# Kernel tuning notes

Measured on AMD Instinct MI355X. Metric: run time of the kernel, lower is better.

Reference implementation:

```python
import jax, jax.numpy as jnp
import numpy as np

B, S, D, H, BLK = 2, 4096, 1024, 16, 64

def setup_inputs() -> dict:
    key = jax.random.key(0)
    ks = jax.random.split(key, 6)
    sc = 0.02
    nb = S // BLK
    g_tok = 128
    ng = g_tok // BLK
    n_mid = nb - ng - 2
    return {
        "tokens": jax.random.normal(ks[0], (B, S, D), dtype=jnp.float32),
        "band_mask": jnp.ones((B, 1, n_mid, BLK, 3 * BLK), dtype=jnp.float32),
        "from_mask": jnp.ones((B, 1, S, 1), dtype=jnp.float32),
        "to_mask": jnp.ones((B, 1, 1, S), dtype=jnp.float32),
        "Wq": jax.random.normal(ks[1], (D, D), dtype=jnp.float32) * sc,
        "Wk": jax.random.normal(ks[2], (D, D), dtype=jnp.float32) * sc,
        "Wv": jax.random.normal(ks[3], (D, D), dtype=jnp.float32) * sc,
        "Wu": jax.random.normal(ks[4], (D, D), dtype=jnp.float32) * sc,
        "bu": jnp.zeros((D,), dtype=jnp.float32),
        "num_global_tokens": 128,
    }

def _forward(tokens, band_mask, from_mask, to_mask, Wq, Wk, Wv, Wu, bu, g):
    b, s, dm = tokens.shape
    h, blk = H, BLK
    d = dm // h
    nb = s // blk
    ng = g // blk
    rs = 1.0 / (d ** 0.5)
    pen = -10000.0

    def heads(x):
        return x.reshape(b, s, h, d).transpose(0, 2, 1, 3)  # (b,h,s,d)

    q = heads(tokens @ Wq)
    k = heads(tokens @ Wk)
    v = heads(tokens @ Wv)
    bq = q.reshape(b, h, nb, blk, d)
    bk = k.reshape(b, h, nb, blk, d)
    bv = v.reshape(b, h, nb, blk, d)

    # --- global (first) block rows: attend to everything ---
    fp = jnp.einsum('bhqd,bhkd->bhqk', q[:, :, :g], k) * rs + (1.0 - to_mask) * pen
    fw = jax.nn.softmax(fp, axis=-1)
    first = jnp.einsum('bhqk,bhkd->bhqd', fw, v).reshape(b, h, ng, blk, d)

    # --- second block: global keys + first 3 non-global blocks ---
    q1 = min(3, nb - ng)
    st = ng * blk
    k2 = jnp.concatenate([k[:, :, :g], k[:, :, st:st + q1 * blk]], axis=2)
    v2 = jnp.concatenate([v[:, :, :g], v[:, :, st:st + q1 * blk]], axis=2)
    p2 = jnp.einsum('bhqd,bhkd->bhqk', bq[:, :, ng], k2) * rs
    p2 = p2 + (1.0 - to_mask[:, :, :, :blk * (ng + q1)]) * pen
    c2 = jnp.einsum('bhqk,bhkd->bhqd', jax.nn.softmax(p2, axis=-1), v2)[:, :, None]

    # --- middle blocks: sliding window (prev, self, next) + global keys ---
    m = nb - ng - 2
    ek = jnp.concatenate([bk[:, :, ng:ng + m], bk[:, :, ng + 1:ng + 1 + m],
                          bk[:, :, ng + 2:ng + 2 + m]], axis=3)  # (b,h,m,3*blk,d)
    ev = jnp.concatenate([bv[:, :, ng:ng + m], bv[:, :, ng + 1:ng + 1 + m],
                          bv[:, :, ng + 2:ng + 2 + m]], axis=3)
    mq = bq[:, :, ng + 1:ng + 1 + m]  # (b,h,m,blk,d)
    inner = jnp.einsum('bhmqd,bhmkd->bhmqk', mq, ek) * rs + (1.0 - band_mask) * pen
    fb = jnp.einsum('bhmqd,bhkd->bhmqk', mq, k[:, :, :g]) * rs
    fb = fb + (1.0 - to_mask[:, :, :, :g][:, :, :, None, :]) * pen
    aw = jax.nn.softmax(jnp.concatenate([fb, inner], axis=-1), axis=-1)
    cm = (jnp.einsum('bhmqk,bhmkd->bhmqd', aw[..., g:], ev)
          + jnp.einsum('bhmqk,bhkd->bhmqd', aw[..., :g], v[:, :, :g]))

    # --- last block: global keys + last 3 blocks ---
    ql = min(3, nb - ng)
    kl = jnp.concatenate([k[:, :, :g], k[:, :, -(ql * blk):]], axis=2)
    vl = jnp.concatenate([v[:, :, :g], v[:, :, -(ql * blk):]], axis=2)
    lm = jnp.concatenate([to_mask[:, :, :, :g], to_mask[:, :, :, -(ql * blk):]], axis=3)
    pl = jnp.einsum('bhqd,bhkd->bhqk', bq[:, :, -1], kl) * rs + (1.0 - lm) * pen
    cl = jnp.einsum('bhqk,bhkd->bhqd', jax.nn.softmax(pl, axis=-1), vl)[:, :, None]

    ctx = jnp.concatenate([first, c2, cm, cl], axis=2).reshape(b, h, s, d) * from_mask
    ctx = ctx.transpose(0, 2, 1, 3).reshape(b, s, dm)
    return ctx @ Wu + bu

def reference(tokens, band_mask, from_mask, to_mask, Wq, Wk, Wv, Wu, bu, num_global_tokens):
    return _forward(tokens, band_mask, from_mask, to_mask, Wq, Wk, Wv, Wu, bu, num_global_tokens)
```

## Files before the change

### kernel.cpp

```cpp
#include <hip/hip_runtime.h>

typedef unsigned short u16;
using bfrag = __attribute__((ext_vector_type(8))) short;
using f32x4 = __attribute__((ext_vector_type(4))) float;

#define PEN  (-10000.0f)
#define RSC  (0.125f)

__device__ __forceinline__ u16 f2bf(float f) {
  union { float f; unsigned u; } v; v.f = f;
  unsigned r = v.u + 0x7fffu + ((v.u >> 16) & 1u);
  return (u16)(r >> 16);
}

__device__ __forceinline__ void gload16(const u16* g, u16* l) {
  __builtin_amdgcn_global_load_lds(
      (const __attribute__((address_space(1))) unsigned int*)g,
      (__attribute__((address_space(3))) unsigned int*)l, 16, 0, 0);
}

__global__ __launch_bounds__(256) void prep_k(
    const float* __restrict__ tokens, u16* __restrict__ tok_bf,
    const float* __restrict__ w0, const float* __restrict__ w1,
    const float* __restrict__ w2, const float* __restrict__ w3,
    u16* __restrict__ wt) {
  __shared__ float tile[64][65];
  int id = blockIdx.x, t = threadIdx.x;
  if (id < 8192) {
    int i = id * 256 + t;
    float4 v = ((const float4*)tokens)[i];
    u16 o[4] = { f2bf(v.x), f2bf(v.y), f2bf(v.z), f2bf(v.w) };
    *(uint2*)(tok_bf + (size_t)i * 4) = *(uint2*)o;
    return;
  }
  int wid = id - 8192;
  int z = wid >> 8, rem = wid & 255;
  const float* W = (z == 0) ? w0 : (z == 1) ? w1 : (z == 2) ? w2 : w3;
  u16* out = wt + (size_t)z * 1024 * 1024;
  int k0 = (rem & 15) * 64, n0 = (rem >> 4) * 64;
#pragma unroll
  for (int i = 0; i < 16; ++i) {
    int idx = i * 256 + t, kk = idx >> 6, nn = idx & 63;
    tile[nn][kk] = W[(size_t)(k0 + kk) * 1024 + n0 + nn];
  }
  __syncthreads();
#pragma unroll
  for (int i = 0; i < 16; ++i) {
    int idx = i * 256 + t, nn = idx >> 6, kk = idx & 63;
    out[(size_t)(n0 + nn) * 1024 + k0 + kk] = f2bf(tile[nn][kk]);
  }
}

__global__ __launch_bounds__(256) void gemm_qkv_k(
    const u16* __restrict__ A, const u16* __restrict__ WT,
    u16* __restrict__ Q, u16* __restrict__ K, u16* __restrict__ VT) {
  __shared__ alignas(16) u16 smem[17408];
  u16* As = smem;
  u16* Bs = smem + 8192;
  int t = threadIdx.x;
  int n0 = blockIdx.x * 128, r0 = blockIdx.y * 128;
  int wave = t >> 6, lane = t & 63, quad = lane >> 4, lcol = lane & 15;
  int wr = wave & 1, wc = wave >> 1;
  int rsel = lane >> 3;
  int sseg = (lane & 7) ^ rsel;
  f32x4 acc[4][4];
#pragma unroll
  for (int mt = 0; mt < 4; ++mt)
#pragma unroll
    for (int nt = 0; nt < 4; ++nt) acc[mt][nt] = (f32x4){0.f, 0.f, 0.f, 0.f};

  const u16* a0 = A + (size_t)r0 * 1024 + sseg * 8;
  const u16* b0 = WT + (size_t)n0 * 1024 + sseg * 8;
  int sw = lcol & 7;

  for (int kt = 0; kt < 16; ++kt) {
#pragma unroll
    for (int i = 0; i < 4; ++i) {
      int ii = wave * 4 + i;
      int row = ii * 8 + rsel;
      gload16(a0 + (size_t)row * 1024 + kt * 64, As + ii * 512);
      gload16(b0 + (size_t)row * 1024 + kt * 64, Bs + ii * 512);
    }
    __syncthreads();
#pragma unroll
    for (int kh = 0; kh < 2; ++kh) {
      int seg = ((kh * 4 + quad) ^ sw) * 8;
      bfrag af[4], bf[4];
#pragma unroll
      for (int x = 0; x < 4; ++x) {
        af[x] = *(const bfrag*)(As + (wr * 64 + x * 16 + lcol) * 64 + seg);
        bf[x] = *(const bfrag*)(Bs + (wc * 64 + x * 16 + lcol) * 64 + seg);
      }
#pragma unroll
      for (int mt = 0; mt < 4; ++mt)
#pragma unroll
        for (int nt = 0; nt < 4; ++nt)
          acc[mt][nt] = __builtin_amdgcn_mfma_f32_16x16x32_bf16(af[mt], bf[nt], acc[mt][nt], 0, 0, 0);
    }
    __syncthreads();
  }
  u16 (*Cs)[136] = (u16(*)[136])smem;
#pragma unroll
  for (int mt = 0; mt < 4; ++mt)
#pragma unroll
    for (int nt = 0; nt < 4; ++nt)
#pragma unroll
      for (int r = 0; r < 4; ++r)
        Cs[wr * 64 + mt * 16 + quad * 4 + r][wc * 64 + nt * 16 + lcol] = f2bf(acc[mt][nt][r]);
  __syncthreads();
  int which = n0 >> 10;
  int b = r0 >> 12, s0v = r0 & 4095;
  if (which < 2) {
    int row = t >> 1, seg = t & 1;
    int h = ((n0 & 1023) >> 6) + seg;
    u16* outp = (which == 0 ? Q : K) + (((size_t)(b * 16 + h) * 4096 + s0v + row) << 6);
#pragma unroll
    for (int jj = 0; jj < 8; ++jj)
      *(uint4*)(outp + jj * 8) = *(uint4*)&Cs[row][seg * 64 + jj * 8];
  } else {
    int c = t & 127, h = ((n0 & 1023) >> 6) + (c >> 6), d = c & 63;
    u16* vtrow = VT + ((size_t)(b * 16 + h) << 18) + ((size_t)d << 12) + s0v;
    int sgb = t >> 7;
#pragma unroll
    for (int i = 0; i < 8; ++i) {
      int sg = sgb + 2 * i;
      u16 tmp[8];
#pragma unroll
      for (int rr = 0; rr < 8; ++rr) tmp[rr] = Cs[sg * 8 + rr][c];
      *(uint4*)(vtrow + sg * 8) = *(uint4*)tmp;
    }
  }
}

__global__ __launch_bounds__(256) void attn_band_k(
    const u16* __restrict__ Qg, const u16* __restrict__ Kg, const u16* __restrict__ VTg,
    const float* __restrict__ band_mask, const float* __restrict__ from_mask,
    const float* __restrict__ to_mask, u16* __restrict__ ctx) {
  __shared__ alignas(16) u16 Qs[64][72];
  __shared__ alignas(16) u16 Ks[64][72];
  __shared__ alignas(16) u16 VTs[64][72];
  __shared__ alignas(16) u16 Ps[64][72];

  int t = threadIdx.x;
  int wave = t >> 6, lane = t & 63, quad = lane >> 4, lcol = lane & 15;
  int j = blockIdx.x + 2, bh = blockIdx.y, b = bh >> 4;

  const u16* qsrc = Qg + (((size_t)bh * 4096 + j * 64) << 6);
#pragma unroll
  for (int i = 0; i < 2; ++i) {
    int idx = i * 256 + t, row = idx >> 3, c8 = (idx & 7) << 3;
    *(uint4*)&Qs[row][c8] = *(const uint4*)(qsrc + row * 64 + c8);
  }
  __syncthreads();
  bfrag qf[2];
#pragma unroll
  for (int kh = 0; kh < 2; ++kh)
    qf[kh] = *(const bfrag*)&Qs[wave * 16 + lcol][kh * 32 + quad * 8];

  float l_part[4] = {0.f, 0.f, 0.f, 0.f};
  f32x4 oa[4];
#pragma unroll
  for (int nt = 0; nt < 4; ++nt) oa[nt] = (f32x4){0.f, 0.f, 0.f, 0.f};

  int sb = (j == 2) ? 2 : ((j == 63) ? 61 : j - 1);

  for (int it = 0; it < 5; ++it) {
    int kb = (it < 2) ? it : (sb + it - 2);
    const u16* ksrc = Kg + (((size_t)bh * 4096 + kb * 64) << 6);
    const u16* vsrc = VTg + ((size_t)bh << 18) + kb * 64;
#pragma unroll
    for (int i = 0; i < 2; ++i) {
      int idx = i * 256 + t, row = idx >> 3, c8 = (idx & 7) << 3;
      *(uint4*)&Ks[row][c8] = *(const uint4*)(ksrc + row * 64 + c8);
      *(uint4*)&VTs[row][c8] = *(const uint4*)(vsrc + ((size_t)row << 12) + c8);
    }
    __syncthreads();

    f32x4 sc[4];
#pragma unroll
    for (int nt = 0; nt < 4; ++nt) sc[nt] = (f32x4){0.f, 0.f, 0.f, 0.f};
#pragma unroll
    for (int kh = 0; kh < 2; ++kh) {
      int kc = kh * 32 + quad * 8;
#pragma unroll
      for (int nt = 0; nt < 4; ++nt) {
        bfrag kf = *(const bfrag*)&Ks[nt * 16 + lcol][kc];
        sc[nt] = __builtin_amdgcn_mfma_f32_16x16x32_bf16(qf[kh], kf, sc[nt], 0, 0, 0);
      }
    }

    bool band = (j >= 3) && (j <= 62) && (it >= 2);
    if (!band) {
#pragma unroll
      for (int nt = 0; nt < 4; ++nt) {
        float tm = to_mask[b * 4096 + kb * 64 + nt * 16 + lcol];
        float pn = (1.0f - tm) * PEN;
#pragma unroll
        for (int r = 0; r < 4; ++r) {
          float p = __expf(sc[nt][r] * RSC + pn);
          l_part[r] += p;
          Ps[wave * 16 + quad * 4 + r][nt * 16 + lcol] = f2bf(p);
        }
      }
    } else {
      const float* bm = band_mask + (((size_t)b * 60 + (j - 3)) << 6) * 192 + (it - 2) * 64;
#pragma unroll
      for (int r = 0; r < 4; ++r) {
        int qrow = wave * 16 + quad * 4 + r;
#pragma unroll
        for (int nt = 0; nt < 4; ++nt) {
          float msk = bm[(size_t)qrow * 192 + nt * 16 + lcol];
          float p = __expf(sc[nt][r] * RSC + (1.0f - msk) * PEN);
          l_part[r] += p;
          Ps[qrow][nt * 16 + lcol] = f2bf(p);
        }
      }
    }
    __syncthreads();

#pragma unroll
    for (int kh = 0; kh < 2; ++kh) {
      bfrag pf = *(const bfrag*)&Ps[wave * 16 + lcol][kh * 32 + quad * 8];
#pragma unroll
      for (int nt = 0; nt < 4; ++nt) {
        bfrag vf = *(const bfrag*)&VTs[nt * 16 + lcol][kh * 32 + quad * 8];
        oa[nt] = __builtin_amdgcn_mfma_f32_16x16x32_bf16(pf, vf, oa[nt], 0, 0, 0);
      }
    }
    __syncthreads();
  }

  float sc_r[4];
#pragma unroll
  for (int r = 0; r < 4; ++r) {
#pragma unroll
    for (int d = 1; d < 16; d <<= 1) l_part[r] += __shfl_xor(l_part[r], d);
    int qrow = wave * 16 + quad * 4 + r;
    sc_r[r] = from_mask[b * 4096 + j * 64 + qrow] / l_part[r];
  }
#pragma unroll
  for (int nt = 0; nt < 4; ++nt)
#pragma unroll
    for (int r = 0; r < 4; ++r)
      Qs[wave * 16 + quad * 4 + r][nt * 16 + lcol] = f2bf(oa[nt][r] * sc_r[r]);
  __syncthreads();
  u16* dst = ctx + (((size_t)bh * 4096 + j * 64) << 6);
#pragma unroll
  for (int i = 0; i < 2; ++i) {
    int idx = i * 256 + t, row = idx >> 3, c8 = (idx & 7) << 3;
    *(uint4*)(dst + row * 64 + c8) = *(uint4*)&Qs[row][c8];
  }
}

__global__ __launch_bounds__(256) void attn_global_k(
    const u16* __restrict__ Qg, const u16* __restrict__ Kg, const u16* __restrict__ VTg,
    const float* __restrict__ to_mask,
    float* __restrict__ Opart, float* __restrict__ lbuf) {
  __shared__ alignas(16) u16 Qs[64][72];
  __shared__ alignas(16) u16 Ks[64][72];
  __shared__ alignas(16) u16 VTs[64][72];
  __shared__ alignas(16) u16 Ps[64][72];

  int t = threadIdx.x;
  int wave = t >> 6, lane = t & 63, quad = lane >> 4, lcol = lane & 15;
  int jc = blockIdx.x, j = jc >> 3, chunk = jc & 7;
  int bh = blockIdx.y, b = bh >> 4;

  const u16* qsrc = Qg + (((size_t)bh * 4096 + j * 64) << 6);
#pragma unroll
  for (int i = 0; i < 2; ++i) {
    int idx = i * 256 + t, row = idx >> 3, c8 = (idx & 7) << 3;
    *(uint4*)&Qs[row][c8] = *(const uint4*)(qsrc + row * 64 + c8);
  }
  __syncthreads();
  bfrag qf[2];
#pragma unroll
  for (int kh = 0; kh < 2; ++kh)
    qf[kh] = *(const bfrag*)&Qs[wave * 16 + lcol][kh * 32 + quad * 8];

  float l_part[4] = {0.f, 0.f, 0.f, 0.f};
  f32x4 oa[4];
#pragma unroll
  for (int nt = 0; nt < 4; ++nt) oa[nt] = (f32x4){0.f, 0.f, 0.f, 0.f};

  for (int it = 0; it < 8; ++it) {
    int kb = chunk * 8 + it;
    const u16* ksrc = Kg + (((size_t)bh * 4096 + kb * 64) << 6);
    const u16* vsrc = VTg + ((size_t)bh << 18) + kb * 64;
#pragma unroll
    for (int i = 0; i < 2; ++i) {
      int idx = i * 256 + t, row = idx >> 3, c8 = (idx & 7) << 3;
      *(uint4*)&Ks[row][c8] = *(const uint4*)(ksrc + row * 64 + c8);
      *(uint4*)&VTs[row][c8] = *(const uint4*)(vsrc + ((size_t)row << 12) + c8);
    }
    __syncthreads();

    f32x4 sc[4];
#pragma unroll
    for (int nt = 0; nt < 4; ++nt) sc[nt] = (f32x4){0.f, 0.f, 0.f, 0.f};
#pragma unroll
    for (int kh = 0; kh < 2; ++kh) {
      int kc = kh * 32 + quad * 8;
#pragma unroll
      for (int nt = 0; nt < 4; ++nt) {
        bfrag kf = *(const bfrag*)&Ks[nt * 16 + lcol][kc];
        sc[nt] = __builtin_amdgcn_mfma_f32_16x16x32_bf16(qf[kh], kf, sc[nt], 0, 0, 0);
      }
    }

#pragma unroll
    for (int nt = 0; nt < 4; ++nt) {
      float tm = to_mask[b * 4096 + kb * 64 + nt * 16 + lcol];
      float pn = (1.0f - tm) * PEN;
#pragma unroll
      for (int r = 0; r < 4; ++r) {
        float p = __expf(sc[nt][r] * RSC + pn);
        l_part[r] += p;
        Ps[wave * 16 + quad * 4 + r][nt * 16 + lcol] = f2bf(p);
      }
    }
    __syncthreads();

#pragma unroll
    for (int kh = 0; kh < 2; ++kh) {
      bfrag pf = *(const bfrag*)&Ps[wave * 16 + lcol][kh * 32 + quad * 8];
#pragma unroll
      for (int nt = 0; nt < 4; ++nt) {
        bfrag vf = *(const bfrag*)&VTs[nt * 16 + lcol][kh * 32 + quad * 8];
        oa[nt] = __builtin_amdgcn_mfma_f32_16x16x32_bf16(pf, vf, oa[nt], 0, 0, 0);
      }
    }
    __syncthreads();
  }

  size_t base = (((size_t)(bh * 2 + j) * 8 + chunk) << 6);
#pragma unroll
  for (int nt = 0; nt < 4; ++nt)
#pragma unroll
    for (int r = 0; r < 4; ++r) {
      int row = wave * 16 + quad * 4 + r;
      Opart[((base + row) << 6) + nt * 16 + lcol] = oa[nt][r];
    }
#pragma unroll
  for (int r = 0; r < 4; ++r) {
#pragma unroll
    for (int d = 1; d < 16; d <<= 1) l_part[r] += __shfl_xor(l_part[r], d);
  }
  if (lcol == 0) {
#pragma unroll
    for (int r = 0; r < 4; ++r) {
      int row = wave * 16 + quad * 4 + r;
      lbuf[base + row] = l_part[r];
    }
  }
}

__global__ __launch_bounds__(256) void attn_combine_k(
    const float* __restrict__ Opart, const float* __restrict__ lbuf,
    const float* __restrict__ from_mask, u16* __restrict__ ctx) {
  int blk = blockIdx.x;
  int bh = blk >> 1, j = blk & 1, b = bh >> 4;
  int t = threadIdx.x;
  int row = t >> 2, dseg = (t & 3) << 4;

  float lt = 0.0f;
  float acc[16];
#pragma unroll
  for (int u = 0; u < 16; ++u) acc[u] = 0.0f;
#pragma unroll
  for (int c = 0; c < 8; ++c) {
    size_t rbase = (((size_t)blk * 8 + c) << 6) + row;
    lt += lbuf[rbase];
    const float* op = Opart + (rbase << 6) + dseg;
#pragma unroll
    for (int u = 0; u < 4; ++u) {
      float4 v = *(const float4*)(op + u * 4);
      acc[u * 4 + 0] += v.x;
      acc[u * 4 + 1] += v.y;
      acc[u * 4 + 2] += v.z;
      acc[u * 4 + 3] += v.w;
    }
  }
  float inv = from_mask[b * 4096 + j * 64 + row] / lt;
  u16* dst = ctx + (((size_t)bh * 4096 + j * 64 + row) << 6) + dseg;
  u16 o[8];
#pragma unroll
  for (int u = 0; u < 8; ++u) o[u] = f2bf(acc[u] * inv);
  *(uint4*)dst = *(uint4*)o;
#pragma unroll
  for (int u = 0; u < 8; ++u) o[u] = f2bf(acc[8 + u] * inv);
  *(uint4*)(dst + 8) = *(uint4*)o;
}

__global__ __launch_bounds__(256) void gemm_out_k(
    const u16* __restrict__ ctx, const u16* __restrict__ WTu,
    const float* __restrict__ bu, float* __restrict__ out) {
  __shared__ alignas(16) u16 smem[16384];
  u16* As = smem;
  u16* Bs = smem + 8192;
  int t = threadIdx.x;
  int n0 = blockIdx.x * 128, r0 = blockIdx.y * 128;
  int wave = t >> 6, lane = t & 63, quad = lane >> 4, lcol = lane & 15;
  int wr = wave & 1, wc = wave >> 1;
  int b = r0 >> 12, s0 = r0 & 4095;
  int rsel = lane >> 3;
  int sseg = (lane & 7) ^ rsel;
  int sw = lcol & 7;
  f32x4 acc[4][4];
#pragma unroll
  for (int mt = 0; mt < 4; ++mt)
#pragma unroll
    for (int nt = 0; nt < 4; ++nt) acc[mt][nt] = (f32x4){0.f, 0.f, 0.f, 0.f};

  const u16* b0 = WTu + (size_t)n0 * 1024 + sseg * 8;
  for (int kt = 0; kt < 16; ++kt) {
    const u16* a0 = ctx + (((size_t)(b * 16 + kt) * 4096 + s0) << 6) + sseg * 8;
#pragma unroll
    for (int i = 0; i < 4; ++i) {
      int ii = wave * 4 + i;
      int row = ii * 8 + rsel;
      gload16(a0 + (size_t)row * 64, As + ii * 512);
      gload16(b0 + (size_t)row * 1024 + kt * 64, Bs + ii * 512);
    }
    __syncthreads();
#pragma unroll
    for (int kh = 0; kh < 2; ++kh) {
      int seg = ((kh * 4 + quad) ^ sw) * 8;
      bfrag af[4], bf[4];
#pragma unroll
      for (int x = 0; x < 4; ++x) {
        af[x] = *(const bfrag*)(As + (wr * 64 + x * 16 + lcol) * 64 + seg);
        bf[x] = *(const bfrag*)(Bs + (wc * 64 + x * 16 + lcol) * 64 + seg);
      }
#pragma unroll
      for (int mt = 0; mt < 4; ++mt)
#pragma unroll
        for (int nt = 0; nt < 4; ++nt)
          acc[mt][nt] = __builtin_amdgcn_mfma_f32_16x16x32_bf16(af[mt], bf[nt], acc[mt][nt], 0, 0, 0);
    }
    __syncthreads();
  }
#pragma unroll
  for (int nt = 0; nt < 4; ++nt) {
    int n = n0 + wc * 64 + nt * 16 + lcol;
    float bv = bu[n];
#pragma unroll
    for (int mt = 0; mt < 4; ++mt)
#pragma unroll
      for (int r = 0; r < 4; ++r)
        out[(size_t)(r0 + wr * 64 + mt * 16 + quad * 4 + r) * 1024 + n] = acc[mt][nt][r] + bv;
  }
}

extern "C" void kernel_launch(void* const* d_in, const int* in_sizes, int n_in,
                              void* d_out, int out_size, void* d_ws, size_t ws_size,
                              hipStream_t stream) {
  const float* tokens    = (const float*)d_in[0];
  const float* band_mask = (const float*)d_in[1];
  const float* from_mask = (const float*)d_in[2];
  const float* to_mask   = (const float*)d_in[3];
  const float* Wq = (const float*)d_in[4];
  const float* Wk = (const float*)d_in[5];
  const float* Wv = (const float*)d_in[6];
  const float* Wu = (const float*)d_in[7];
  const float* bu = (const float*)d_in[8];
  float* out = (float*)d_out;

  char* ws = (char*)d_ws;
  u16* tok_bf = (u16*)(ws);
  u16* WT     = (u16*)(ws + 16777216);
  u16* Qb     = (u16*)(ws + 16777216 + 8388608);
  u16* Kb     = Qb + 8388608;
  u16* VTb    = Kb + 8388608;
  u16* ctx    = VTb + 8388608;
  float* Opart = (float*)(ctx + 8388608);
  float* lb    = Opart + (size_t)32 * 2 * 8 * 64 * 64;

  prep_k<<<9216, 256, 0, stream>>>(tokens, tok_bf, Wq, Wk, Wv, Wu, WT);
  gemm_qkv_k<<<dim3(24, 64), 256, 0, stream>>>(tok_bf, WT, Qb, Kb, VTb);
  attn_band_k<<<dim3(62, 32), 256, 0, stream>>>(Qb, Kb, VTb, band_mask, from_mask, to_mask, ctx);
  attn_global_k<<<dim3(16, 32), 256, 0, stream>>>(Qb, Kb, VTb, to_mask, Opart, lb);
  attn_combine_k<<<64, 256, 0, stream>>>(Opart, lb, from_mask, ctx);
  gemm_out_k<<<dim3(8, 64), 256, 0, stream>>>(ctx, WT + (size_t)3 * 1024 * 1024, bu, out);
}
```

Before: 261.7 us.

## Merge band and global attention kernels with double-buffered async K/V loads

Fuses the band and global attention kernels into a single launch, choosing the role from the block index. K and V^T tiles are now double-buffered and fetched with global_load_lds direct-to-LDS loads so the next tile streams in while the current one is computed. Shared memory uses an XOR swizzle instead of padding, and the Q and P buffers share one allocation. This removes a kernel launch and the load stall at each iteration, at the cost of more complex indexing and extra LDS for the second buffer.

```diff
diff --git a/kernel.cpp b/kernel.cpp
--- a/kernel.cpp
+++ b/kernel.cpp
@@ -132,65 +132,92 @@
   }
 }
 
-__global__ __launch_bounds__(256) void attn_band_k(
+__global__ __launch_bounds__(256) void attn_k(
     const u16* __restrict__ Qg, const u16* __restrict__ Kg, const u16* __restrict__ VTg,
     const float* __restrict__ band_mask, const float* __restrict__ from_mask,
-    const float* __restrict__ to_mask, u16* __restrict__ ctx) {
-  __shared__ alignas(16) u16 Qs[64][72];
-  __shared__ alignas(16) u16 Ks[64][72];
-  __shared__ alignas(16) u16 VTs[64][72];
-  __shared__ alignas(16) u16 Ps[64][72];
+    const float* __restrict__ to_mask, u16* __restrict__ ctx,
+    float* __restrict__ Opart, float* __restrict__ lbuf) {
+  __shared__ alignas(16) u16 QPs[4096];
+  __shared__ alignas(16) u16 Ks[2][4096];
+  __shared__ alignas(16) u16 VTs[2][4096];
 
   int t = threadIdx.x;
   int wave = t >> 6, lane = t & 63, quad = lane >> 4, lcol = lane & 15;
-  int j = blockIdx.x + 2, bh = blockIdx.y, b = bh >> 4;
-
-  const u16* qsrc = Qg + (((size_t)bh * 4096 + j * 64) << 6);
-#pragma unroll
-  for (int i = 0; i < 2; ++i) {
-    int idx = i * 256 + t, row = idx >> 3, c8 = (idx & 7) << 3;
-    *(uint4*)&Qs[row][c8] = *(const uint4*)(qsrc + row * 64 + c8);
-  }
+  int rsel = lane >> 3, sseg = (lane & 7) ^ rsel;
+  int sw = lcol & 7;
+  int bh = blockIdx.y, b = bh >> 4;
+  bool is_band = blockIdx.x < 62;
+  int j, chunk = 0, nit, sb = 0;
+  if (is_band) {
+    j = blockIdx.x + 2; nit = 5;
+    sb = (j == 2) ? 2 : ((j == 63) ? 61 : j - 1);
+  } else {
+    int jc = blockIdx.x - 62; j = jc >> 3; chunk = jc & 7; nit = 8;
+  }
+  bool bandmask_blk = is_band && (j >= 3) && (j <= 62);
+
+  const u16* kbase = Kg + (((size_t)bh * 4096) << 6) + sseg * 8;
+  const u16* vbase = VTg + ((size_t)bh << 18) + sseg * 8;
+
+  auto kb_of = [&](int it) {
+    return is_band ? ((it < 2) ? it : (sb + it - 2)) : (chunk * 8 + it);
+  };
+  auto stage = [&](int kb, int buf) {
+#pragma unroll
+    for (int i = 0; i < 2; ++i) {
+      int ii = wave * 2 + i;
+      int row = ii * 8 + rsel;
+      gload16(kbase + (((size_t)kb * 64 + row) << 6), &Ks[buf][ii * 512]);
+      gload16(vbase + ((size_t)row << 12) + kb * 64, &VTs[buf][ii * 512]);
+    }
+  };
+
+  {
+    const u16* qsrc = Qg + (((size_t)bh * 4096 + j * 64) << 6) + sseg * 8;
+#pragma unroll
+    for (int i = 0; i < 2; ++i) {
+      int ii = wave * 2 + i;
+      gload16(qsrc + (ii * 8 + rsel) * 64, &QPs[ii * 512]);
+    }
+  }
+  stage(kb_of(0), 0);
   __syncthreads();
+
   bfrag qf[2];
 #pragma unroll
   for (int kh = 0; kh < 2; ++kh)
-    qf[kh] = *(const bfrag*)&Qs[wave * 16 + lcol][kh * 32 + quad * 8];
+    qf[kh] = *(const bfrag*)&QPs[(wave * 16 + lcol) * 64 + ((kh * 4 + quad) ^ sw) * 8];
+  __syncthreads();
 
   float l_part[4] = {0.f, 0.f, 0.f, 0.f};
   f32x4 oa[4];
 #pragma unroll
   for (int nt = 0; nt < 4; ++nt) oa[nt] = (f32x4){0.f, 0.f, 0.f, 0.f};
 
-  int sb = (j == 2) ? 2 : ((j == 63) ? 61 : j - 1);
-
-  for (int it = 0; it < 5; ++it) {
-    int kb = (it < 2) ? it : (sb + it - 2);
-    const u16* ksrc = Kg + (((size_t)bh * 4096 + kb * 64) << 6);
-    const u16* vsrc = VTg + ((size_t)bh << 18) + kb * 64;
-#pragma unroll
-    for (int i = 0; i < 2; ++i) {
-      int idx = i * 256 + t, row = idx >> 3, c8 = (idx & 7) << 3;
-      *(uint4*)&Ks[row][c8] = *(const uint4*)(ksrc + row * 64 + c8);
-      *(uint4*)&VTs[row][c8] = *(const uint4*)(vsrc + ((size_t)row << 12) + c8);
-    }
-    __syncthreads();
+  int poff = lcol & 7;
+  int hb = lcol >> 3;
+  int q1_4 = (quad & 1) * 4;
+
+  for (int it = 0; it < nit; ++it) {
+    int buf = it & 1;
+    if (it + 1 < nit) stage(kb_of(it + 1), buf ^ 1);
+    int kb = kb_of(it);
 
     f32x4 sc[4];
 #pragma unroll
     for (int nt = 0; nt < 4; ++nt) sc[nt] = (f32x4){0.f, 0.f, 0.f, 0.f};
 #pragma unroll
     for (int kh = 0; kh < 2; ++kh) {
-      int kc = kh * 32 + quad * 8;
+      int seg = ((kh * 4 + quad) ^ sw) * 8;
 #pragma unroll
       for (int nt = 0; nt < 4; ++nt) {
-        bfrag kf = *(const bfrag*)&Ks[nt * 16 + lcol][kc];
+        bfrag kf = *(const bfrag*)&Ks[buf][(nt * 16 + lcol) * 64 + seg];
         sc[nt] = __builtin_amdgcn_mfma_f32_16x16x32_bf16(qf[kh], kf, sc[nt], 0, 0, 0);
       }
     }
 
-    bool band = (j >= 3) && (j <= 62) && (it >= 2);
-    if (!band) {
+    bool use_band = bandmask_blk && (it >= 2);
+    if (!use_band) {
 #pragma unroll
       for (int nt = 0; nt < 4; ++nt) {
         float tm = to_mask[b * 4096 + kb * 64 + nt * 16 + lcol];
@@ -199,7 +226,8 @@
         for (int r = 0; r < 4; ++r) {
           float p = __expf(sc[nt][r] * RSC + pn);
           l_part[r] += p;
-          Ps[wave * 16 + quad * 4 + r][nt * 16 + lcol] = f2bf(p);
+          int pseg = (nt * 2 + hb) ^ (q1_4 + r);
+          QPs[(wave * 16 + quad * 4 + r) * 64 + pseg * 8 + poff] = f2bf(p);
         }
       }
     } else {
@@ -212,7 +240,8 @@
           float msk = bm[(size_t)qrow * 192 + nt * 16 + lcol];
           float p = __expf(sc[nt][r] * RSC + (1.0f - msk) * PEN);
           l_part[r] += p;
-          Ps[qrow][nt * 16 + lcol] = f2bf(p);
+          int pseg = (nt * 2 + hb) ^ (q1_4 + r);
+          QPs[qrow * 64 + pseg * 8 + poff] = f2bf(p);
         }
       }
     }
@@ -220,137 +249,58 @@
 
 #pragma unroll
     for (int kh = 0; kh < 2; ++kh) {
-      bfrag pf = *(const bfrag*)&Ps[wave * 16 + lcol][kh * 32 + quad * 8];
+      int seg = ((kh * 4 + quad) ^ sw) * 8;
+      bfrag pf = *(const bfrag*)&QPs[(wave * 16 + lcol) * 64 + seg];
 #pragma unroll
       for (int nt = 0; nt < 4; ++nt) {
-        bfrag vf = *(const bfrag*)&VTs[nt * 16 + lcol][kh * 32 + quad * 8];
+        bfrag vf = *(const bfrag*)&VTs[buf][(nt * 16 + lcol) * 64 + seg];
         oa[nt] = __builtin_amdgcn_mfma_f32_16x16x32_bf16(pf, vf, oa[nt], 0, 0, 0);
       }
     }
     __syncthreads();
   }
 
-  float sc_r[4];
-#pragma unroll
-  for (int r = 0; r < 4; ++r) {
-#pragma unroll
-    for (int d = 1; d < 16; d <<= 1) l_part[r] += __shfl_xor(l_part[r], d);
-    int qrow = wave * 16 + quad * 4 + r;
-    sc_r[r] = from_mask[b * 4096 + j * 64 + qrow] / l_part[r];
-  }
-#pragma unroll
-  for (int nt = 0; nt < 4; ++nt)
-#pragma unroll
-    for (int r = 0; r < 4; ++r)
-      Qs[wave * 16 + quad * 4 + r][nt * 16 + lcol] = f2bf(oa[nt][r] * sc_r[r]);
-  __syncthreads();
-  u16* dst = ctx + (((size_t)bh * 4096 + j * 64) << 6);
-#pragma unroll
-  for (int i = 0; i < 2; ++i) {
-    int idx = i * 256 + t, row = idx >> 3, c8 = (idx & 7) << 3;
-    *(uint4*)(dst + row * 64 + c8) = *(uint4*)&Qs[row][c8];
-  }
-}
-
-__global__ __launch_bounds__(256) void attn_global_k(
-    const u16* __restrict__ Qg, const u16* __restrict__ Kg, const u16* __restrict__ VTg,
-    const float* __restrict__ to_mask,
-    float* __restrict__ Opart, float* __restrict__ lbuf) {
-  __shared__ alignas(16) u16 Qs[64][72];
-  __shared__ alignas(16) u16 Ks[64][72];
-  __shared__ alignas(16) u16 VTs[64][72];
-  __shared__ alignas(16) u16 Ps[64][72];
-
-  int t = threadIdx.x;
-  int wave = t >> 6, lane = t & 63, quad = lane >> 4, lcol = lane & 15;
-  int jc = blockIdx.x, j = jc >> 3, chunk = jc & 7;
-  int bh = blockIdx.y, b = bh >> 4;
-
-  const u16* qsrc = Qg + (((size_t)bh * 4096 + j * 64) << 6);
-#pragma unroll
-  for (int i = 0; i < 2; ++i) {
-    int idx = i * 256 + t, row = idx >> 3, c8 = (idx & 7) << 3;
-    *(uint4*)&Qs[row][c8] = *(const uint4*)(qsrc + row * 64 + c8);
-  }
-  __syncthreads();
-  bfrag qf[2];
-#pragma unroll
-  for (int kh = 0; kh < 2; ++kh)
-    qf[kh] = *(const bfrag*)&Qs[wave * 16 + lcol][kh * 32 + quad * 8];
-
-  float l_part[4] = {0.f, 0.f, 0.f, 0.f};
-  f32x4 oa[4];
-#pragma unroll
-  for (int nt = 0; nt < 4; ++nt) oa[nt] = (f32x4){0.f, 0.f, 0.f, 0.f};
-
-  for (int it = 0; it < 8; ++it) {
-    int kb = chunk * 8 + it;
-    const u16* ksrc = Kg + (((size_t)bh * 4096 + kb * 64) << 6);
-    const u16* vsrc = VTg + ((size_t)bh << 18) + kb * 64;
+  if (is_band) {
+    float sc_r[4];
+#pragma unroll
+    for (int r = 0; r < 4; ++r) {
+#pragma unroll
+      for (int d = 1; d < 16; d <<= 1) l_part[r] += __shfl_xor(l_part[r], d);
+      int qrow = wave * 16 + quad * 4 + r;
+      sc_r[r] = from_mask[b * 4096 + j * 64 + qrow] / l_part[r];
+    }
+#pragma unroll
+    for (int nt = 0; nt < 4; ++nt)
+#pragma unroll
+      for (int r = 0; r < 4; ++r) {
+        int pseg = (nt * 2 + hb) ^ (q1_4 + r);
+        QPs[(wave * 16 + quad * 4 + r) * 64 + pseg * 8 + poff] = f2bf(oa[nt][r] * sc_r[r]);
+      }
+    __syncthreads();
+    u16* dst = ctx + (((size_t)bh * 4096 + j * 64) << 6);
 #pragma unroll
     for (int i = 0; i < 2; ++i) {
-      int idx = i * 256 + t, row = idx >> 3, c8 = (idx & 7) << 3;
-      *(uint4*)&Ks[row][c8] = *(const uint4*)(ksrc + row * 64 + c8);
-      *(uint4*)&VTs[row][c8] = *(const uint4*)(vsrc + ((size_t)row << 12) + c8);
-    }
-    __syncthreads();
-
-    f32x4 sc[4];
-#pragma unroll
-    for (int nt = 0; nt < 4; ++nt) sc[nt] = (f32x4){0.f, 0.f, 0.f, 0.f};
-#pragma unroll
-    for (int kh = 0; kh < 2; ++kh) {
-      int kc = kh * 32 + quad * 8;
-#pragma unroll
-      for (int nt = 0; nt < 4; ++nt) {
-        bfrag kf = *(const bfrag*)&Ks[nt * 16 + lcol][kc];
-        sc[nt] = __builtin_amdgcn_mfma_f32_16x16x32_bf16(qf[kh], kf, sc[nt], 0, 0, 0);
-      }
-    }
-
-#pragma unroll
-    for (int nt = 0; nt < 4; ++nt) {
-      float tm = to_mask[b * 4096 + kb * 64 + nt * 16 + lcol];
-      float pn = (1.0f - tm) * PEN;
+      int idx = i * 256 + t, row = idx >> 3, s = idx & 7;
+      *(uint4*)(dst + row * 64 + s * 8) = *(uint4*)&QPs[row * 64 + (s ^ (row & 7)) * 8];
+    }
+  } else {
+    size_t base = (((size_t)(bh * 2 + j) * 8 + chunk) << 6);
+#pragma unroll
+    for (int nt = 0; nt < 4; ++nt)
 #pragma unroll
       for (int r = 0; r < 4; ++r) {
-        float p = __expf(sc[nt][r] * RSC + pn);
-        l_part[r] += p;
-        Ps[wave * 16 + quad * 4 + r][nt * 16 + lcol] = f2bf(p);
-      }
-    }
-    __syncthreads();
-
-#pragma unroll
-    for (int kh = 0; kh < 2; ++kh) {
-      bfrag pf = *(const bfrag*)&Ps[wave * 16 + lcol][kh * 32 + quad * 8];
-#pragma unroll
-      for (int nt = 0; nt < 4; ++nt) {
-        bfrag vf = *(const bfrag*)&VTs[nt * 16 + lcol][kh * 32 + quad * 8];
-        oa[nt] = __builtin_amdgcn_mfma_f32_16x16x32_bf16(pf, vf, oa[nt], 0, 0, 0);
-      }
-    }
-    __syncthreads();
-  }
-
-  size_t base = (((size_t)(bh * 2 + j) * 8 + chunk) << 6);
-#pragma unroll
-  for (int nt = 0; nt < 4; ++nt)
+        int row = wave * 16 + quad * 4 + r;
+        Opart[((base + row) << 6) + nt * 16 + lcol] = oa[nt][r];
+      }
 #pragma unroll
     for (int r = 0; r < 4; ++r) {
-      int row = wave * 16 + quad * 4 + r;
-      Opart[((base + row) << 6) + nt * 16 + lcol] = oa[nt][r];
-    }
-#pragma unroll
-  for (int r = 0; r < 4; ++r) {
-#pragma unroll
-    for (int d = 1; d < 16; d <<= 1) l_part[r] += __shfl_xor(l_part[r], d);
-  }
-  if (lcol == 0) {
-#pragma unroll
-    for (int r = 0; r < 4; ++r) {
-      int row = wave * 16 + quad * 4 + r;
-      lbuf[base + row] = l_part[r];
+#pragma unroll
+      for (int d = 1; d < 16; d <<= 1) l_part[r] += __shfl_xor(l_part[r], d);
+    }
+    if (lcol == 0) {
+#pragma unroll
+      for (int r = 0; r < 4; ++r)
+        lbuf[base + wave * 16 + quad * 4 + r] = l_part[r];
     }
   }
 }
@@ -478,8 +428,8 @@
 
   prep_k<<<9216, 256, 0, stream>>>(tokens, tok_bf, Wq, Wk, Wv, Wu, WT);
   gemm_qkv_k<<<dim3(24, 64), 256, 0, stream>>>(tok_bf, WT, Qb, Kb, VTb);
-  attn_band_k<<<dim3(62, 32), 256, 0, stream>>>(Qb, Kb, VTb, band_mask, from_mask, to_mask, ctx);
-  attn_global_k<<<dim3(16, 32), 256, 0, stream>>>(Qb, Kb, VTb, to_mask, Opart, lb);
+  attn_k<<<dim3(78, 32), 256, 0, stream>>>(Qb, Kb, VTb, band_mask, from_mask, to_mask,
+                                           ctx, Opart, lb);
   attn_combine_k<<<64, 256, 0, stream>>>(Opart, lb, from_mask, ctx);
   gemm_out_k<<<dim3(8, 64), 256, 0, stream>>>(ctx, WT + (size_t)3 * 1024 * 1024, bu, out);
 }
```

Result: slower. 268.9 us (+2.8%).
